# Kernel tuning notes

Hardware: AMD Instinct MI355X
Metric: run time of the kernel (lower is better)

## Reference

```python
import jax, jax.numpy as jnp
import numpy as np

D_EMBED = 512
NUM_HEADS = 8
HEAD_DIM = D_EMBED // NUM_HEADS
D_FF = 2048
B, L = 2, 4096
LN_EPS = 1e-5


def _layernorm(x, g, b):
    mu = jnp.mean(x, axis=-1, keepdims=True)
    var = jnp.mean(jnp.square(x - mu), axis=-1, keepdims=True)
    return (x - mu) * jax.lax.rsqrt(var + LN_EPS) * g + b


def setup_inputs() -> dict:
    key = jax.random.key(0)
    ks = jax.random.split(key, 16)
    s = 0.02
    inp = {
        "x": jax.random.normal(ks[0], (B, L, D_EMBED), dtype=jnp.float32),
        "mask": jnp.ones((B, 1, 1, L), dtype=jnp.int32),
        # attention projections (stored [in, out] for x @ W)
        "Wq": jax.random.normal(ks[1], (D_EMBED, D_EMBED), dtype=jnp.float32) * s,
        "bq": jnp.zeros((D_EMBED,), dtype=jnp.float32),
        "Wk": jax.random.normal(ks[2], (D_EMBED, D_EMBED), dtype=jnp.float32) * s,
        "bk": jnp.zeros((D_EMBED,), dtype=jnp.float32),
        "Wv": jax.random.normal(ks[3], (D_EMBED, D_EMBED), dtype=jnp.float32) * s,
        "bv": jnp.zeros((D_EMBED,), dtype=jnp.float32),
        "Wo": jax.random.normal(ks[4], (D_EMBED, D_EMBED), dtype=jnp.float32) * s,
        "bo": jnp.zeros((D_EMBED,), dtype=jnp.float32),
        # layernorms
        "ln1_g": jnp.ones((D_EMBED,), dtype=jnp.float32),
        "ln1_b": jnp.zeros((D_EMBED,), dtype=jnp.float32),
        "ln2_g": jnp.ones((D_EMBED,), dtype=jnp.float32),
        "ln2_b": jnp.zeros((D_EMBED,), dtype=jnp.float32),
        # FFN
        "W1": jax.random.normal(ks[5], (D_EMBED, D_FF), dtype=jnp.float32) * s,
        "b1": jnp.zeros((D_FF,), dtype=jnp.float32),
        "W2": jax.random.normal(ks[6], (D_FF, D_EMBED), dtype=jnp.float32) * s,
        "b2": jnp.zeros((D_EMBED,), dtype=jnp.float32),
    }
    return inp


def reference(x, mask, Wq, bq, Wk, bk, Wv, bv, Wo, bo, ln1_g, ln1_b,
              W1, b1, W2, b2, ln2_g, ln2_b):
    Bx, Lx, _ = x.shape
    # projections -> [B, H, L, Dh]
    def split_heads(t):
        return t.reshape(Bx, Lx, NUM_HEADS, HEAD_DIM).transpose(0, 2, 1, 3)
    q = split_heads(x @ Wq + bq)
    k = split_heads(x @ Wk + bk)
    v = split_heads(x @ Wv + bv)
    scores = jnp.einsum("bhqd,bhkd->bhqk", q, k) / jnp.sqrt(
        jnp.asarray(HEAD_DIM, dtype=x.dtype))
    scores = jnp.where(mask == 0, jnp.asarray(-1e9, dtype=x.dtype), scores)
    attn = jax.nn.softmax(scores, axis=-1)
    ctx = jnp.einsum("bhqk,bhkd->bhqd", attn, v)
    ctx = ctx.transpose(0, 2, 1, 3).reshape(Bx, Lx, D_EMBED)
    attn_out = ctx @ Wo + bo

    h = _layernorm(x + attn_out, ln1_g, ln1_b)
    ff = (jax.nn.gelu(h @ W1 + b1, approximate=False)) @ W2 + b2
    return _layernorm(h + ff, ln2_g, ln2_b)
```

## Files before the change

kernel.cpp:

```cpp
#include <hip/hip_runtime.h>
#include <hip/hip_bf16.h>
#include <math.h>

#define D_EMBED 512
#define NUM_HEADS 8
#define HEAD_DIM 64
#define D_FF 2048
#define BATCH 2
#define SEQ 4096
#define M_ROWS (BATCH*SEQ)
#define QSCALE 0.18033688011112042f

typedef __attribute__((ext_vector_type(8))) short short8;
typedef __attribute__((ext_vector_type(4))) short short4_t;
typedef __attribute__((ext_vector_type(4))) float f32x4;
typedef __attribute__((ext_vector_type(16))) float f32x16;

#if __has_builtin(__builtin_amdgcn_exp2f)
#define EXP2(x) __builtin_amdgcn_exp2f(x)
#else
#define EXP2(x) exp2f(x)
#endif

__device__ inline unsigned short f2b(float f) {
    union { float f; unsigned u; } v; v.f = f;
    unsigned r = v.u + 0x7fffu + ((v.u >> 16) & 1u);
    return (unsigned short)(r >> 16);
}

__device__ inline float b2f(short s) {
    union { unsigned u; float f; } v;
    v.u = ((unsigned)(unsigned short)s) << 16;
    return v.f;
}

__device__ inline short4_t pk4(float p0, float p1, float p2, float p3) {
    union { __hip_bfloat162 h2[2]; short4_t s4; } u;
    u.h2[0] = __float22bfloat162_rn(make_float2(p0, p1));
    u.h2[1] = __float22bfloat162_rn(make_float2(p2, p3));
    return u.s4;
}

__device__ inline unsigned pk2(float lo, float hi) {
    union { __hip_bfloat162 h2; unsigned u; } x;
    x.h2 = __float22bfloat162_rn(make_float2(lo, hi));
    return x.u;
}

__device__ inline void plswap(unsigned a, unsigned b, unsigned &r0, unsigned &r1) {
#if __has_builtin(__builtin_amdgcn_permlane32_swap)
    auto v = __builtin_amdgcn_permlane32_swap(a, b, false, false);
    r0 = (unsigned)v[0]; r1 = (unsigned)v[1];
#else
    unsigned ax = (unsigned)__shfl_xor((int)a, 32, 64);
    unsigned bx = (unsigned)__shfl_xor((int)b, 32, 64);
    bool hi = (threadIdx.x & 32) != 0;
    r0 = hi ? bx : a;
    r1 = hi ? b  : ax;
#endif
}

__device__ inline short8 pfrag8(const float* p) {
    unsigned a0 = pk2(p[0], p[1]), a1 = pk2(p[2], p[3]);
    unsigned b0 = pk2(p[4], p[5]), b1 = pk2(p[6], p[7]);
    unsigned u0, u1, u2, u3;
    plswap(a0, b0, u0, u1);
    plswap(a1, b1, u2, u3);
    union { unsigned u[4]; short8 s; } r;
    r.u[0] = u0; r.u[1] = u2; r.u[2] = u1; r.u[3] = u3;
    return r.s;
}

__device__ inline void gl2lds16(const void* g, void* l) {
    __builtin_amdgcn_global_load_lds(
        (const __attribute__((address_space(1))) unsigned int*)g,
        (__attribute__((address_space(3))) unsigned int*)l, 16, 0, 0);
}

template<int EPI>
__global__ __launch_bounds__(256) void gemm_bt(
    const unsigned short* __restrict__ A, const unsigned short* __restrict__ BT,
    const float* __restrict__ bias, void* __restrict__ Cout,
    int M, int N, int K)
{
    __shared__ __align__(16) unsigned short As[128*32];
    __shared__ __align__(16) unsigned short Bs[128*32];
    const int tid  = threadIdx.x;
    const int wave = tid >> 6, lane = tid & 63;
    const int wy = wave >> 1, wx = wave & 1;
    const int quad = lane >> 4, m16 = lane & 15;
    const int row0 = blockIdx.y * 128, n0 = blockIdx.x * 128;
    const int rdoff = (quad ^ ((m16 >> 1) & 3)) * 8;

    f32x4 acc[4][4];
#pragma unroll
    for (int i = 0; i < 4; i++)
#pragma unroll
        for (int j = 0; j < 4; j++) acc[i][j] = (f32x4){0.f,0.f,0.f,0.f};

    const int kIters = K >> 5;
    for (int kt = 0; kt < kIters; ++kt) {
        const int k0 = kt << 5;
#pragma unroll
        for (int it = 0; it < 2; ++it) {
            int g  = it*256 + tid;
            int r  = g >> 2;
            int c8 = (((g & 3) ^ ((g >> 3) & 3)) << 3);
            gl2lds16(A  + (size_t)(row0 + r)*K + k0 + c8, &As[(size_t)(it*256 + wave*64)*8]);
            gl2lds16(BT + (size_t)(n0  + r)*K + k0 + c8, &Bs[(size_t)(it*256 + wave*64)*8]);
        }
        __syncthreads();
        short8 a[4], b[4];
#pragma unroll
        for (int i = 0; i < 4; i++) a[i] = *(const short8*)&As[(wy*64 + i*16 + m16)*32 + rdoff];
#pragma unroll
        for (int j = 0; j < 4; j++) b[j] = *(const short8*)&Bs[(wx*64 + j*16 + m16)*32 + rdoff];
#pragma unroll
        for (int i = 0; i < 4; i++)
#pragma unroll
            for (int j = 0; j < 4; j++)
                acc[i][j] = __builtin_amdgcn_mfma_f32_16x16x32_bf16(a[i], b[j], acc[i][j], 0, 0, 0);
        __syncthreads();
    }

#pragma unroll
    for (int j = 0; j < 4; j++) {
        int col = n0 + wx*64 + j*16 + m16;
        float bj = bias[col];
#pragma unroll
        for (int i = 0; i < 4; i++) {
            int rbase = row0 + wy*64 + i*16 + quad*4;
#pragma unroll
            for (int r = 0; r < 4; r++) {
                float v = acc[i][j][r] + bj;
                size_t idx = (size_t)(rbase + r)*N + col;
                if (EPI == 0) {
                    ((unsigned short*)Cout)[idx] = f2b(v);
                } else {
                    float gv = 0.5f * v * (1.0f + erff(v * 0.70710678118654752f));
                    ((unsigned short*)Cout)[idx] = f2b(gv);
                }
            }
        }
    }
}

__global__ __launch_bounds__(256) void gemm_qkv(
    const unsigned short* __restrict__ A, const unsigned short* __restrict__ BT,
    const float* __restrict__ bias,
    unsigned short* __restrict__ Qp, unsigned short* __restrict__ Kp,
    unsigned short* __restrict__ Vp)
{
    const int K = 512;
    __shared__ __align__(16) unsigned short As[128*32];
    __shared__ __align__(16) unsigned short Bs[128*32];
    const int tid  = threadIdx.x;
    const int wave = tid >> 6, lane = tid & 63;
    const int wy = wave >> 1, wx = wave & 1;
    const int quad = lane >> 4, m16 = lane & 15;
    const int row0 = blockIdx.y * 128, n0 = blockIdx.x * 128;
    const int rdoff = (quad ^ ((m16 >> 1) & 3)) * 8;
    const int region = n0 >> 9;

    f32x4 acc[4][4];
#pragma unroll
    for (int i = 0; i < 4; i++)
#pragma unroll
        for (int j = 0; j < 4; j++) acc[i][j] = (f32x4){0.f,0.f,0.f,0.f};

    for (int kt = 0; kt < 16; ++kt) {
        const int k0 = kt << 5;
#pragma unroll
        for (int it = 0; it < 2; ++it) {
            int g  = it*256 + tid;
            int r  = g >> 2;
            int c8 = (((g & 3) ^ ((g >> 3) & 3)) << 3);
            gl2lds16(A  + (size_t)(row0 + r)*K + k0 + c8, &As[(size_t)(it*256 + wave*64)*8]);
            gl2lds16(BT + (size_t)(n0  + r)*K + k0 + c8, &Bs[(size_t)(it*256 + wave*64)*8]);
        }
        __syncthreads();
        short8 a[4], b[4];
#pragma unroll
        for (int i = 0; i < 4; i++) a[i] = *(const short8*)&As[(wy*64 + i*16 + m16)*32 + rdoff];
#pragma unroll
        for (int j = 0; j < 4; j++) b[j] = *(const short8*)&Bs[(wx*64 + j*16 + m16)*32 + rdoff];
#pragma unroll
        for (int i = 0; i < 4; i++)
#pragma unroll
            for (int j = 0; j < 4; j++)
                acc[i][j] = __builtin_amdgcn_mfma_f32_16x16x32_bf16(a[i], b[j], acc[i][j], 0, 0, 0);
        __syncthreads();
    }

    const float sc = (region == 0) ? QSCALE : 1.0f;
#pragma unroll
    for (int j = 0; j < 4; j++) {
        int col = n0 + wx*64 + j*16 + m16;
        float bj = bias[col];
        int cc = col & 511, h = cc >> 6, d = cc & 63;
#pragma unroll
        for (int i = 0; i < 4; i++) {
            int rbase = row0 + wy*64 + i*16 + quad*4;
#pragma unroll
            for (int r = 0; r < 4; r++) {
                float v = (acc[i][j][r] + bj) * sc;
                int row = rbase + r;
                int b = row >> 12, l = row & 4095;
                size_t bh = (size_t)(b*8 + h);
                if (region == 0) {
                    Qp[(bh*SEQ + l)*64 + d] = f2b(v);
                } else if (region == 1) {
                    Kp[(bh*SEQ + l)*64 + d] = f2b(v);
                } else {
                    Vp[(bh*64 + d)*SEQ + l] = f2b(v);
                }
            }
        }
    }
}

__global__ __launch_bounds__(256) void gemm_bt64(
    const unsigned short* __restrict__ A, const unsigned short* __restrict__ BT,
    const float* __restrict__ bias, unsigned short* __restrict__ Cout,
    int M, int N, int K)
{
    __shared__ __align__(16) unsigned short As[64*32];
    __shared__ __align__(16) unsigned short Bs[128*32];
    const int tid  = threadIdx.x;
    const int wave = tid >> 6, lane = tid & 63;
    const int wy = wave >> 1, wx = wave & 1;
    const int quad = lane >> 4, m16 = lane & 15;
    const int row0 = blockIdx.y * 64, n0 = blockIdx.x * 128;
    const int rdoff = (quad ^ ((m16 >> 1) & 3)) * 8;

    f32x4 acc[2][4];
#pragma unroll
    for (int i = 0; i < 2; i++)
#pragma unroll
        for (int j = 0; j < 4; j++) acc[i][j] = (f32x4){0.f,0.f,0.f,0.f};

    const int kIters = K >> 5;
    for (int kt = 0; kt < kIters; ++kt) {
        const int k0 = kt << 5;
        {
            int r = tid >> 2;
            int c8 = (((tid & 3) ^ ((tid >> 3) & 3)) << 3);
            gl2lds16(A + (size_t)(row0 + r)*K + k0 + c8, &As[(size_t)(wave*64)*8]);
        }
#pragma unroll
        for (int it = 0; it < 2; ++it) {
            int g  = it*256 + tid;
            int r  = g >> 2;
            int c8 = (((g & 3) ^ ((g >> 3) & 3)) << 3);
            gl2lds16(BT + (size_t)(n0 + r)*K + k0 + c8, &Bs[(size_t)(it*256 + wave*64)*8]);
        }
        __syncthreads();
        short8 a[2], b[4];
#pragma unroll
        for (int i = 0; i < 2; i++) a[i] = *(const short8*)&As[(wy*32 + i*16 + m16)*32 + rdoff];
#pragma unroll
        for (int j = 0; j < 4; j++) b[j] = *(const short8*)&Bs[(wx*64 + j*16 + m16)*32 + rdoff];
#pragma unroll
        for (int i = 0; i < 2; i++)
#pragma unroll
            for (int j = 0; j < 4; j++)
                acc[i][j] = __builtin_amdgcn_mfma_f32_16x16x32_bf16(a[i], b[j], acc[i][j], 0, 0, 0);
        __syncthreads();
    }

#pragma unroll
    for (int j = 0; j < 4; j++) {
        int col = n0 + wx*64 + j*16 + m16;
        float bj = bias[col];
#pragma unroll
        for (int i = 0; i < 2; i++) {
            int rbase = row0 + wy*32 + i*16 + quad*4;
#pragma unroll
            for (int r = 0; r < 4; r++) {
                float v = acc[i][j][r] + bj;
                Cout[(size_t)(rbase + r)*N + col] = f2b(v);
            }
        }
    }
}

__global__ __launch_bounds__(256) void prep(
    const float* __restrict__ Wq, const float* __restrict__ Wk,
    const float* __restrict__ Wv, const float* __restrict__ Wo,
    const float* __restrict__ W1, const float* __restrict__ W2,
    const float* __restrict__ bq, const float* __restrict__ bk,
    const float* __restrict__ bv, const int* __restrict__ mask,
    unsigned short* __restrict__ WqkvT, unsigned short* __restrict__ WoT,
    unsigned short* __restrict__ W1T, unsigned short* __restrict__ W2T,
    float* __restrict__ bqkv, int* __restrict__ mflag, unsigned* __restrict__ kmax2)
{
    const int id = blockIdx.x, t = threadIdx.x;
    if (id == 3072) {
        if (t < 64) {
            const int* m = mask + t*128;
            int all = 1;
            for (int i = 0; i < 128; i += 4) {
                int4 v = *(const int4*)(m + i);
                all &= (v.x && v.y && v.z && v.w) ? 1 : 0;
            }
            mflag[t] = all;
        }
        if (t < 16) kmax2[t] = 0u;
        for (int i = t; i < 1536; i += 256)
            bqkv[i] = (i < 512) ? bq[i] : ((i < 1024) ? bk[i-512] : bv[i-1024]);
        return;
    }
    __shared__ float tt[32][33];
    const float* W; unsigned short* WT; int K, N, bx, by;
    if (id < 256)       { W = Wq; WT = WqkvT;            K = 512;  N = 512;  bx = id & 15;  by = id >> 4; }
    else if (id < 512)  { int l = id - 256;  W = Wk; WT = WqkvT + 512*512;  K = 512;  N = 512;  bx = l & 15; by = l >> 4; }
    else if (id < 768)  { int l = id - 512;  W = Wv; WT = WqkvT + 1024*512; K = 512;  N = 512;  bx = l & 15; by = l >> 4; }
    else if (id < 1024) { int l = id - 768;  W = Wo; WT = WoT;              K = 512;  N = 512;  bx = l & 15; by = l >> 4; }
    else if (id < 2048) { int l = id - 1024; W = W1; WT = W1T;              K = 512;  N = 2048; bx = l & 63; by = l >> 6; }
    else                { int l = id - 2048; W = W2; WT = W2T;              K = 2048; N = 512;  bx = l & 15; by = l >> 4; }
    const int n0 = bx*32, k0 = by*32;
    const int x = t & 31, y = t >> 5;
#pragma unroll
    for (int yy = y; yy < 32; yy += 8) tt[yy][x] = W[(size_t)(k0+yy)*N + n0 + x];
    __syncthreads();
#pragma unroll
    for (int yy = y; yy < 32; yy += 8) WT[(size_t)(n0+yy)*K + k0 + x] = f2b(tt[x][yy]);
}

__global__ __launch_bounds__(256) void kmax_k(
    const unsigned short* __restrict__ Kp, unsigned* __restrict__ kmax2)
{
    const int bh = blockIdx.x, t = threadIdx.x;
    const int row = blockIdx.y*256 + t;
    const unsigned short* kp = Kp + ((size_t)bh*SEQ + row)*64;
    float s = 0.f;
#pragma unroll
    for (int c = 0; c < 8; ++c) {
        short8 v = *(const short8*)(kp + c*8);
#pragma unroll
        for (int j = 0; j < 8; ++j) { float f = b2f(v[j]); s += f*f; }
    }
#pragma unroll
    for (int off = 32; off >= 1; off >>= 1)
        s = fmaxf(s, __shfl_xor(s, off, 64));
    if ((t & 63) == 0) atomicMax(&kmax2[bh], __float_as_uint(s));
}

__global__ __launch_bounds__(512, 2) void flash_attn(
    const unsigned short* __restrict__ Qp, const unsigned short* __restrict__ Kp,
    const unsigned short* __restrict__ Vt, const int* __restrict__ mask,
    const int* __restrict__ flags, const unsigned* __restrict__ kmax2,
    unsigned short* __restrict__ O)
{
    __shared__ __align__(16) unsigned short Ks[2][128*64];
    __shared__ __align__(16) unsigned short Vs[2][64*128];
    __shared__ float rsp[8][64];
    const int tid = threadIdx.x, wave = tid >> 6, lane = tid & 63;
    const int qsub = wave & 3, kp = wave >> 2;
    const int c = lane & 31, l5 = lane >> 5;
    const int bh = blockIdx.y, b = bh >> 3, h = bh & 7;
    const int qbase = blockIdx.x * 128 + qsub * 32;

    const unsigned short* Qb = Qp + (size_t)bh*SEQ*64;
    const unsigned short* Kb = Kp + (size_t)bh*SEQ*64;
    const unsigned short* Vb = Vt + (size_t)bh*64*SEQ;
    const int* mbase = mask + b*SEQ;
    const int* fbase = flags + b*(SEQ/128);
    const float kmx = __uint_as_float(kmax2[bh]);

    short8 qf[4];
    float Mq;
    {
        const unsigned short* qp = Qb + (size_t)(qbase + c)*64 + l5*8;
        float qn2 = 0.f;
#pragma unroll
        for (int t = 0; t < 4; ++t) {
            qf[t] = *(const short8*)(qp + t*16);
#pragma unroll
            for (int j = 0; j < 8; ++j) { float f = b2f(qf[t][j]); qn2 += f*f; }
        }
        qn2 += __shfl_xor(qn2, 32, 64);
        Mq = sqrtf(qn2 * kmx);
    }

    f32x16 accO[2];
#pragma unroll
    for (int dg = 0; dg < 2; ++dg)
#pragma unroll
        for (int r = 0; r < 16; ++r) accO[dg][r] = 0.f;
    float rs = 0.f;

#define STAGE(nb, ktn) do {                                                   \
        const int key0s = (ktn)*128;                                          \
        _Pragma("unroll")                                                     \
        for (int it = 0; it < 2; ++it) {                                      \
            int idx = it*512 + tid;                                           \
            int r = idx >> 3, chn = idx & 7;                                  \
            gl2lds16(Kb + (size_t)(key0s + r)*64 + ((chn ^ (r & 7)) << 3),    \
                     &Ks[nb][(it*512 + wave*64)*8]);                          \
        }                                                                     \
        _Pragma("unroll")                                                     \
        for (int it = 0; it < 2; ++it) {                                      \
            int idx = it*512 + tid;                                           \
            int r = idx >> 4, chn = idx & 15;                                 \
            gl2lds16(Vb + (size_t)r*SEQ + key0s + ((chn ^ (r & 15)) << 3),    \
                     &Vs[nb][(it*512 + wave*64)*8]);                          \
        }                                                                     \
    } while (0)

    STAGE(0, 0);
    __syncthreads();
    int cb = 0;
    const int NT = SEQ/128;

    for (int kt = 0; kt < NT; ++kt) {
        if (kt + 1 < NT) STAGE(cb ^ 1, kt + 1);
        const int allones = fbase[kt];
        const int key0 = kt * 128;
        const unsigned short* Kt  = Ks[cb];
        const unsigned short* Vtl = Vs[cb];

#pragma unroll
        for (int g = 0; g < 2; ++g) {
            const int kg = kp*2 + g;
            short8 kf[4];
#pragma unroll
            for (int t = 0; t < 4; ++t) {
                int row = kg*32 + c;
                int chn = (t*2 + l5) ^ (row & 7);
                kf[t] = *(const short8*)&Kt[row*64 + chn*8];
            }
            f32x16 s;
#pragma unroll
            for (int r = 0; r < 16; ++r) s[r] = -Mq;
#pragma unroll
            for (int t = 0; t < 4; ++t)
                s = __builtin_amdgcn_mfma_f32_32x32x16_bf16(kf[t], qf[t], s, 0, 0, 0);
            if (!allones) {
#pragma unroll
                for (int r = 0; r < 16; ++r) {
                    int mv = mbase[key0 + kg*32 + (r & 3) + 8*(r >> 2) + 4*l5];
                    if (!mv) s[r] = -1e9f;
                }
            }
            float pa[16];
#pragma unroll
            for (int r = 0; r < 16; ++r) pa[r] = EXP2(s[r]);
            rs += (((pa[0]+pa[1])+(pa[2]+pa[3])) + ((pa[4]+pa[5])+(pa[6]+pa[7])))
                + (((pa[8]+pa[9])+(pa[10]+pa[11])) + ((pa[12]+pa[13])+(pa[14]+pa[15])));

            short8 vf[2][2];
#pragma unroll
            for (int c2 = 0; c2 < 2; ++c2)
#pragma unroll
                for (int dg = 0; dg < 2; ++dg) {
                    int row = dg*32 + c;
                    int chn = ((kg*2 + c2)*2 + l5) ^ (row & 15);
                    vf[c2][dg] = *(const short8*)&Vtl[row*128 + chn*8];
                }
#pragma unroll
            for (int c2 = 0; c2 < 2; ++c2) {
                short8 pf = pfrag8(&pa[c2*8]);
                accO[0] = __builtin_amdgcn_mfma_f32_32x32x16_bf16(vf[c2][0], pf, accO[0], 0, 0, 0);
                accO[1] = __builtin_amdgcn_mfma_f32_32x32x16_bf16(vf[c2][1], pf, accO[1], 0, 0, 0);
            }
        }
        __syncthreads();
        cb ^= 1;
    }
#undef STAGE

    float* const ksf = (float*)&Ks[0][0];
    rsp[wave][lane] = rs;
    float* mp = ksf + qsub*2048;
    if (kp == 1) {
#pragma unroll
        for (int dg = 0; dg < 2; ++dg)
#pragma unroll
            for (int r = 0; r < 16; ++r)
                mp[(dg*16 + r)*64 + lane] = accO[dg][r];
    }
    __syncthreads();
    if (kp == 0) {
#pragma unroll
        for (int dg = 0; dg < 2; ++dg)
#pragma unroll
            for (int r = 0; r < 16; ++r)
                accO[dg][r] += mp[(dg*16 + r)*64 + lane];
        rs += rsp[4 + qsub][lane];

        rs += __shfl_xor(rs, 32, 64);
        float rl = 1.0f / rs;
        int qrow = qbase + c;
        unsigned short* op = O + (size_t)(b*SEQ + qrow)*D_EMBED + h*HEAD_DIM;
#pragma unroll
        for (int dg = 0; dg < 2; ++dg)
#pragma unroll
            for (int q4 = 0; q4 < 4; ++q4) {
                short4_t o = pk4(accO[dg][q4*4+0]*rl, accO[dg][q4*4+1]*rl,
                                 accO[dg][q4*4+2]*rl, accO[dg][q4*4+3]*rl);
                *(short4_t*)&op[dg*32 + q4*8 + l5*4] = o;
            }
    }
}

__global__ __launch_bounds__(256) void ln_res1(
    const float* __restrict__ A, const unsigned short* __restrict__ Bv,
    const float* __restrict__ g, const float* __restrict__ be,
    unsigned short* __restrict__ Yb)
{
    const int wave = threadIdx.x >> 6, lane = threadIdx.x & 63;
    const int row = blockIdx.x * 4 + wave;
    const float* ap = A + (size_t)row*512 + lane*8;
    short8 bv = *(const short8*)(Bv + (size_t)row*512 + lane*8);
    float v[8]; float s = 0.f;
#pragma unroll
    for (int j = 0; j < 8; j++) { v[j] = ap[j] + b2f(bv[j]); s += v[j]; }
#pragma unroll
    for (int off = 32; off >= 1; off >>= 1) s += __shfl_xor(s, off, 64);
    float mu = s * (1.f/512.f);
    float q = 0.f;
#pragma unroll
    for (int j = 0; j < 8; j++) { v[j] -= mu; q += v[j]*v[j]; }
#pragma unroll
    for (int off = 32; off >= 1; off >>= 1) q += __shfl_xor(q, off, 64);
    float rstd = rsqrtf(q * (1.f/512.f) + 1e-5f);
#pragma unroll
    for (int j = 0; j < 8; j++) {
        float y = v[j]*rstd*g[lane*8+j] + be[lane*8+j];
        Yb[(size_t)row*512 + lane*8 + j] = f2b(y);
    }
}

__global__ __launch_bounds__(256) void ln_res2(
    const unsigned short* __restrict__ A, const unsigned short* __restrict__ Bv,
    const float* __restrict__ g, const float* __restrict__ be,
    float* __restrict__ Yf)
{
    const int wave = threadIdx.x >> 6, lane = threadIdx.x & 63;
    const int row = blockIdx.x * 4 + wave;
    short8 av = *(const short8*)(A  + (size_t)row*512 + lane*8);
    short8 bv = *(const short8*)(Bv + (size_t)row*512 + lane*8);
    float v[8]; float s = 0.f;
#pragma unroll
    for (int j = 0; j < 8; j++) { v[j] = b2f(av[j]) + b2f(bv[j]); s += v[j]; }
#pragma unroll
    for (int off = 32; off >= 1; off >>= 1) s += __shfl_xor(s, off, 64);
    float mu = s * (1.f/512.f);
    float q = 0.f;
#pragma unroll
    for (int j = 0; j < 8; j++) { v[j] -= mu; q += v[j]*v[j]; }
#pragma unroll
    for (int off = 32; off >= 1; off >>= 1) q += __shfl_xor(q, off, 64);
    float rstd = rsqrtf(q * (1.f/512.f) + 1e-5f);
#pragma unroll
    for (int j = 0; j < 8; j++) {
        float y = v[j]*rstd*g[lane*8+j] + be[lane*8+j];
        Yf[(size_t)row*512 + lane*8 + j] = y;
    }
}

__global__ __launch_bounds__(256) void cvt_f32_bf16(
    const float* __restrict__ X, unsigned short* __restrict__ Y, int n)
{
    int idx = (blockIdx.x * 256 + threadIdx.x) * 4;
    if (idx < n) {
        float4 v = *(const float4*)(X + idx);
        Y[idx+0] = f2b(v.x); Y[idx+1] = f2b(v.y);
        Y[idx+2] = f2b(v.z); Y[idx+3] = f2b(v.w);
    }
}

extern "C" void kernel_launch(void* const* d_in, const int* in_sizes, int n_in,
                              void* d_out, int out_size, void* d_ws, size_t ws_size,
                              hipStream_t stream)
{
    const float* x    = (const float*)d_in[0];
    const int*   mask = (const int*)  d_in[1];
    const float* Wq = (const float*)d_in[2];  const float* bq = (const float*)d_in[3];
    const float* Wk = (const float*)d_in[4];  const float* bk = (const float*)d_in[5];
    const float* Wv = (const float*)d_in[6];  const float* bv = (const float*)d_in[7];
    const float* Wo = (const float*)d_in[8];  const float* bo = (const float*)d_in[9];
    const float* ln1g = (const float*)d_in[10]; const float* ln1b = (const float*)d_in[11];
    const float* ln2g = (const float*)d_in[12]; const float* ln2b = (const float*)d_in[13];
    const float* W1 = (const float*)d_in[14]; const float* b1 = (const float*)d_in[15];
    const float* W2 = (const float*)d_in[16]; const float* b2 = (const float*)d_in[17];
    float* out = (float*)d_out;

    char* ws = (char*)d_ws;
    const size_t MB = 1024*1024;
    unsigned short* xb    = (unsigned short*)(ws + 0);
    unsigned short* WqkvT = (unsigned short*)(ws + 8*MB);
    unsigned short* W1T   = (unsigned short*)(ws + 10*MB);
    unsigned short* W2T   = (unsigned short*)(ws + 12*MB);
    unsigned short* WoT   = (unsigned short*)(ws + 14*MB);
    float*          bqkv  = (float*)(ws + 14*MB + 512*1024);
    int*            mflag = (int*)(ws + 14*MB + 768*1024);
    unsigned*       kmaxb = (unsigned*)(ws + 14*MB + 772*1024);
    unsigned short* Qp    = (unsigned short*)(ws + 15*MB);
    unsigned short* Kp    = (unsigned short*)(ws + 23*MB);
    unsigned short* Vp    = (unsigned short*)(ws + 31*MB);
    unsigned short* ctx   = (unsigned short*)(ws + 39*MB);
    unsigned short* atfb  = (unsigned short*)(ws + 47*MB);
    unsigned short* hb    = (unsigned short*)(ws + 0);
    unsigned short* Gb    = (unsigned short*)(ws + 15*MB);
    unsigned short* ffb   = (unsigned short*)(ws + 47*MB);

    cvt_f32_bf16<<<4096, 256, 0, stream>>>(x, xb, M_ROWS*D_EMBED);
    prep<<<3073, 256, 0, stream>>>(Wq, Wk, Wv, Wo, W1, W2, bq, bk, bv, mask,
                                   WqkvT, WoT, W1T, W2T, bqkv, mflag, kmaxb);

    gemm_qkv<<<dim3(12,64), 256, 0, stream>>>(xb, WqkvT, bqkv, Qp, Kp, Vp);

    kmax_k<<<dim3(16,16), 256, 0, stream>>>(Kp, kmaxb);
    flash_attn<<<dim3(SEQ/128, 16), 512, 0, stream>>>(Qp, Kp, Vp, mask, mflag, kmaxb, ctx);

    gemm_bt64<<<dim3(4,128), 256, 0, stream>>>(ctx, WoT, bo, atfb, M_ROWS, 512, 512);
    ln_res1<<<M_ROWS/4, 256, 0, stream>>>(x, atfb, ln1g, ln1b, hb);

    gemm_bt<2><<<dim3(16,64), 256, 0, stream>>>(hb, W1T, b1, Gb, M_ROWS, D_FF, 512);
    gemm_bt64<<<dim3(4,128), 256, 0, stream>>>(Gb, W2T, b2, ffb, M_ROWS, 512, D_FF);
    ln_res2<<<M_ROWS/4, 256, 0, stream>>>(hb, ffb, ln2g, ln2b, out);
}
```

Before: 375.8 us.

## Shrink flash-attention blocks to 64 queries with single-buffered K/V and MFMA priority

The flash-attention kernel now uses 256-thread blocks covering 64 queries each, so the grid has twice as many blocks. It drops the double-buffered K/V LDS staging in favour of a single buffer loaded between two barriers per key tile. The launch bound allows four resident blocks per CU, and `s_setprio` raises wave priority around the MFMA sequences. The aim is to hide memory latency through more independent blocks rather than intra-block prefetch. The cost is twice the total K/V loads from L2 and an exposed load stall per tile inside each block. The mask-flag computation is split into two per-batch thread ranges with the same result.

```diff
diff --git a/kernel.cpp b/kernel.cpp
--- a/kernel.cpp
+++ b/kernel.cpp
@@ -296,7 +296,7 @@
 {
     const int id = blockIdx.x, t = threadIdx.x;
     if (id == 3072) {
-        if (t < 64) {
+        if (t < 32) {
             const int* m = mask + t*128;
             int all = 1;
             for (int i = 0; i < 128; i += 4) {
@@ -304,6 +304,14 @@
                 all &= (v.x && v.y && v.z && v.w) ? 1 : 0;
             }
             mflag[t] = all;
+        } else if (t >= 64 && t < 96) {
+            const int* m = mask + SEQ + (t - 64)*128;
+            int all = 1;
+            for (int i = 0; i < 128; i += 4) {
+                int4 v = *(const int4*)(m + i);
+                all &= (v.x && v.y && v.z && v.w) ? 1 : 0;
+            }
+            mflag[32 + (t - 64)] = all;
         }
         if (t < 16) kmax2[t] = 0u;
         for (int i = t; i < 1536; i += 256)
@@ -346,20 +354,20 @@
     if ((t & 63) == 0) atomicMax(&kmax2[bh], __float_as_uint(s));
 }
 
-__global__ __launch_bounds__(512, 2) void flash_attn(
+__global__ __launch_bounds__(256, 4) void flash_attn(
     const unsigned short* __restrict__ Qp, const unsigned short* __restrict__ Kp,
     const unsigned short* __restrict__ Vt, const int* __restrict__ mask,
     const int* __restrict__ flags, const unsigned* __restrict__ kmax2,
     unsigned short* __restrict__ O)
 {
-    __shared__ __align__(16) unsigned short Ks[2][128*64];
-    __shared__ __align__(16) unsigned short Vs[2][64*128];
-    __shared__ float rsp[8][64];
+    __shared__ __align__(16) unsigned short Ks[128*64];
+    __shared__ __align__(16) unsigned short Vs[64*128];
+    __shared__ float rsp[4][64];
     const int tid = threadIdx.x, wave = tid >> 6, lane = tid & 63;
-    const int qsub = wave & 3, kp = wave >> 2;
+    const int qsub = wave & 1, kp = wave >> 1;
     const int c = lane & 31, l5 = lane >> 5;
     const int bh = blockIdx.y, b = bh >> 3, h = bh & 7;
-    const int qbase = blockIdx.x * 128 + qsub * 32;
+    const int qbase = blockIdx.x * 64 + qsub * 32;
 
     const unsigned short* Qb = Qp + (size_t)bh*SEQ*64;
     const unsigned short* Kb = Kp + (size_t)bh*SEQ*64;
@@ -390,36 +398,27 @@
         for (int r = 0; r < 16; ++r) accO[dg][r] = 0.f;
     float rs = 0.f;
 
-#define STAGE(nb, ktn) do {                                                   \
-        const int key0s = (ktn)*128;                                          \
-        _Pragma("unroll")                                                     \
-        for (int it = 0; it < 2; ++it) {                                      \
-            int idx = it*512 + tid;                                           \
-            int r = idx >> 3, chn = idx & 7;                                  \
-            gl2lds16(Kb + (size_t)(key0s + r)*64 + ((chn ^ (r & 7)) << 3),    \
-                     &Ks[nb][(it*512 + wave*64)*8]);                          \
-        }                                                                     \
-        _Pragma("unroll")                                                     \
-        for (int it = 0; it < 2; ++it) {                                      \
-            int idx = it*512 + tid;                                           \
-            int r = idx >> 4, chn = idx & 15;                                 \
-            gl2lds16(Vb + (size_t)r*SEQ + key0s + ((chn ^ (r & 15)) << 3),    \
-                     &Vs[nb][(it*512 + wave*64)*8]);                          \
-        }                                                                     \
-    } while (0)
-
-    STAGE(0, 0);
-    __syncthreads();
-    int cb = 0;
     const int NT = SEQ/128;
-
     for (int kt = 0; kt < NT; ++kt) {
-        if (kt + 1 < NT) STAGE(cb ^ 1, kt + 1);
+        const int key0 = kt * 128;
+        __syncthreads();
+#pragma unroll
+        for (int it = 0; it < 4; ++it) {
+            int idx = it*256 + tid;
+            int r = idx >> 3, chn = idx & 7;
+            gl2lds16(Kb + (size_t)(key0 + r)*64 + ((chn ^ (r & 7)) << 3),
+                     &Ks[(it*256 + wave*64)*8]);
+        }
+#pragma unroll
+        for (int it = 0; it < 4; ++it) {
+            int idx = it*256 + tid;
+            int r = idx >> 4, chn = idx & 15;
+            gl2lds16(Vb + (size_t)r*SEQ + key0 + ((chn ^ (r & 15)) << 3),
+                     &Vs[(it*256 + wave*64)*8]);
+        }
+        __syncthreads();
+
         const int allones = fbase[kt];
-        const int key0 = kt * 128;
-        const unsigned short* Kt  = Ks[cb];
-        const unsigned short* Vtl = Vs[cb];
-
 #pragma unroll
         for (int g = 0; g < 2; ++g) {
             const int kg = kp*2 + g;
@@ -428,14 +427,16 @@
             for (int t = 0; t < 4; ++t) {
                 int row = kg*32 + c;
                 int chn = (t*2 + l5) ^ (row & 7);
-                kf[t] = *(const short8*)&Kt[row*64 + chn*8];
+                kf[t] = *(const short8*)&Ks[row*64 + chn*8];
             }
             f32x16 s;
 #pragma unroll
             for (int r = 0; r < 16; ++r) s[r] = -Mq;
+            __builtin_amdgcn_s_setprio(1);
 #pragma unroll
             for (int t = 0; t < 4; ++t)
                 s = __builtin_amdgcn_mfma_f32_32x32x16_bf16(kf[t], qf[t], s, 0, 0, 0);
+            __builtin_amdgcn_s_setprio(0);
             if (!allones) {
 #pragma unroll
                 for (int r = 0; r < 16; ++r) {
@@ -456,21 +457,22 @@
                 for (int dg = 0; dg < 2; ++dg) {
                     int row = dg*32 + c;
                     int chn = ((kg*2 + c2)*2 + l5) ^ (row & 15);
-                    vf[c2][dg] = *(const short8*)&Vtl[row*128 + chn*8];
+                    vf[c2][dg] = *(const short8*)&Vs[row*128 + chn*8];
                 }
 #pragma unroll
             for (int c2 = 0; c2 < 2; ++c2) {
                 short8 pf = pfrag8(&pa[c2*8]);
+                __builtin_amdgcn_s_setprio(1);
                 accO[0] = __builtin_amdgcn_mfma_f32_32x32x16_bf16(vf[c2][0], pf, accO[0], 0, 0, 0);
                 accO[1] = __builtin_amdgcn_mfma_f32_32x32x16_bf16(vf[c2][1], pf, accO[1], 0, 0, 0);
-            }
-        }
-        __syncthreads();
-        cb ^= 1;
-    }
-#undef STAGE
-
-    float* const ksf = (float*)&Ks[0][0];
+                __builtin_amdgcn_s_setprio(0);
+            }
+        }
+    }
+
+    __syncthreads();
+
+    float* const ksf = (float*)&Ks[0];
     rsp[wave][lane] = rs;
     float* mp = ksf + qsub*2048;
     if (kp == 1) {
@@ -487,7 +489,7 @@
 #pragma unroll
             for (int r = 0; r < 16; ++r)
                 accO[dg][r] += mp[(dg*16 + r)*64 + lane];
-        rs += rsp[4 + qsub][lane];
+        rs += rsp[2 + qsub][lane];
 
         rs += __shfl_xor(rs, 32, 64);
         float rl = 1.0f / rs;
@@ -613,7 +615,7 @@
     gemm_qkv<<<dim3(12,64), 256, 0, stream>>>(xb, WqkvT, bqkv, Qp, Kp, Vp);
 
     kmax_k<<<dim3(16,16), 256, 0, stream>>>(Kp, kmaxb);
-    flash_attn<<<dim3(SEQ/128, 16), 512, 0, stream>>>(Qp, Kp, Vp, mask, mflag, kmaxb, ctx);
+    flash_attn<<<dim3(SEQ/64, 16), 256, 0, stream>>>(Qp, Kp, Vp, mask, mflag, kmaxb, ctx);
 
     gemm_bt64<<<dim3(4,128), 256, 0, stream>>>(ctx, WoT, bo, atfb, M_ROWS, 512, 512);
     ln_res1<<<M_ROWS/4, 256, 0, stream>>>(x, atfb, ln1g, ln1b, hb);
```

Result: slower. 438.9 us (+16.8%).
